# Performance work log

Measured on AMD Instinct MI355X. Metric: run time of the kernel, lower is better.

## Reference

```python
import math
import jax, jax.numpy as jnp
import numpy as np

HID = 256; NH = 8; DH = 32; DFF = 1024  # int(4.0*256)
N = 10000; E = 160000; NV = 128; NG = 64


def _ln(x, eps=1e-6):
    m = jnp.mean(x, axis=-1, keepdims=True)
    v = jnp.mean((x - m) ** 2, axis=-1, keepdims=True)
    return (x - m) * jax.lax.rsqrt(v + eps)


def _modulate(x, shift, scale):
    return x * (1.0 + scale) + shift


def _swiglu(x, W12, Wout):
    a, b = jnp.split(x @ W12, 2, axis=-1)
    return (jax.nn.silu(a) * b) @ Wout


def _adaln(t, W, b):
    return jnp.split(jax.nn.silu(t) @ W + b, 6, axis=-1)


def setup_inputs() -> dict:
    key = jax.random.key(0)
    ks = jax.random.split(key, 32)
    rn = lambda k, shape, s=1.0: jax.random.normal(k, shape, jnp.float32) * s
    W = 0.02
    return {
        "batch": jnp.sort(jax.random.randint(ks[0], (N,), 0, NG)),
        "x": rn(ks[1], (N, HID)),
        "t_emb_h": rn(ks[2], (N, HID)),
        "edge_attr": rn(ks[3], (E, HID)),
        "edge_index": jax.random.randint(ks[4], (2, E), 0, N),
        "t_emb_e": rn(ks[5], (E, HID)),
        "dist": rn(ks[6], (E, NV)),
        "W_edge_emb": rn(ks[7], (HID + NV, HID), W),
        "b_edge_emb": jnp.zeros((HID,), jnp.float32),
        "W_adaln": rn(ks[8], (HID, 6 * HID), W),
        "b_adaln": jnp.zeros((6 * HID,), jnp.float32),
        "W_adaln_e": rn(ks[9], (HID, 6 * HID), W),
        "b_adaln_e": jnp.zeros((6 * HID,), jnp.float32),
        "W_qkv": rn(ks[10], (HID, 3 * HID), W),
        "W_e0": rn(ks[11], (HID, HID), W),
        "W_e1": rn(ks[12], (HID, HID), W),
        "W_n2e": rn(ks[13], (HID, HID), W),
        "b_n2e": jnp.zeros((HID,), jnp.float32),
        "g_ln": jnp.ones((HID,), jnp.float32),
        "b_ln": jnp.zeros((HID,), jnp.float32),
        "W_ffn12": rn(ks[14], (HID, 2 * DFF), W),
        "W_ffn_out": rn(ks[15], (DFF, HID), W),
        "W_ffne12": rn(ks[16], (HID, 2 * DFF), W),
        "W_ffne_out": rn(ks[17], (DFF, HID), W),
    }


def reference(batch, x, t_emb_h, edge_attr, edge_index, t_emb_e, dist,
              W_edge_emb, b_edge_emb, W_adaln, b_adaln, W_adaln_e, b_adaln_e,
              W_qkv, W_e0, W_e1, W_n2e, b_n2e, g_ln, b_ln,
              W_ffn12, W_ffn_out, W_ffne12, W_ffne_out):
    src, tgt = edge_index[0], edge_index[1]
    n = x.shape[0]
    h_in_node = x
    h_in_edge = edge_attr

    shift_msa, scale_msa, gate_msa, shift_mlp, scale_mlp, gate_mlp = _adaln(t_emb_h, W_adaln, b_adaln)
    e_shift_msa, e_scale_msa, e_gate_msa, e_shift_mlp, e_scale_mlp, e_gate_mlp = _adaln(t_emb_e, W_adaln_e, b_adaln_e)

    edge_attr_e = jnp.concatenate([edge_attr, dist], axis=-1) @ W_edge_emb + b_edge_emb
    x_mod = _modulate(_ln(x), shift_msa, scale_msa)
    prev_edge_attr = edge_attr_e
    e_mod = _modulate(_ln(edge_attr_e), e_shift_msa, e_scale_msa)

    qkv = x_mod @ W_qkv                         # N x 3H
    Q, K, V = jnp.split(qkv, 3, axis=-1)
    Q = Q.reshape(-1, NH, DH)
    K = K.reshape(-1, NH, DH)
    V = V.reshape(-1, NH, DH)

    query_i = Q[src]                            # E x NH x DH
    key_j = K[tgt]
    value_j = V[tgt]
    edge_attn = jax.nn.gelu(e_mod @ W_e0, approximate=True).reshape(-1, NH, DH)

    alpha = jnp.sum(query_i * key_j * edge_attn, axis=-1) / math.sqrt(DH)  # E x NH
    # segment softmax over edges grouped by target node
    amax = jax.ops.segment_max(alpha, tgt, num_segments=n)                 # N x NH
    exp_a = jnp.exp(alpha - amax[tgt])
    denom = jax.ops.segment_sum(exp_a, tgt, num_segments=n)
    alpha = exp_a / denom[tgt]

    msg = value_j * (e_mod @ W_e1).reshape(-1, NH, DH) * alpha[..., None]
    out = jax.ops.segment_sum(msg.reshape(-1, NH * DH), tgt, num_segments=n)  # N x H

    h_node = out
    h_edge = (h_node[src] + h_node[tgt]) @ W_n2e + b_n2e

    h_node = h_in_node + gate_msa * h_node
    h_node = _modulate(_ln(h_node) * g_ln + b_ln, shift_mlp, scale_mlp)
    h_out = h_node + gate_mlp * _swiglu(h_node, W_ffn12, W_ffn_out)

    h_edge = h_in_edge + e_gate_msa * h_edge
    h_edge = _modulate(_ln(h_edge), e_shift_mlp, e_scale_mlp)
    h_edge_out = prev_edge_attr + h_edge + e_gate_mlp * _swiglu(h_edge, W_ffne12, W_ffne_out)
    return (h_out, h_edge_out)
```

## Files before the change

kernel.cpp:

```cpp
#include <hip/hip_runtime.h>

#define HID 256

typedef unsigned short u16;
typedef __attribute__((ext_vector_type(8))) short bf16x8;
typedef __attribute__((ext_vector_type(4))) float f32x4;

__device__ __forceinline__ float siluf(float x) { return x / (1.f + __expf(-x)); }
__device__ __forceinline__ float geluf(float x) {
    return x / (1.f + __expf(-(1.59576912f * x + 0.07135481f * x * x * x)));
}
__device__ __forceinline__ u16 f2b(float x) {
    unsigned u = __float_as_uint(x);
    unsigned r = u + 0x7FFFu + ((u >> 16) & 1u);
    return (u16)(r >> 16);
}
__device__ __forceinline__ float b2f(u16 h) {
    return __uint_as_float(((unsigned)h) << 16);
}
__device__ __forceinline__ void gload16(const u16* g, u16* l) {
    __builtin_amdgcn_global_load_lds(
        (const __attribute__((address_space(1))) unsigned int*)g,
        (__attribute__((address_space(3))) unsigned int*)l, 16, 0, 0);
}
__device__ __forceinline__ int imin(int a, int b) { return a < b ? a : b; }

__global__ __launch_bounds__(256) void gemm_mfma(
    const u16* __restrict__ A, int lda,
    const u16* __restrict__ Bt, int ldb,
    void* __restrict__ Cv, int ldc,
    int M, int N, int K,
    const float* __restrict__ bias, int act, int obf16)
{
    __shared__ u16 lds[8192];

    const int tid  = threadIdx.x;
    const int lane = tid & 63;
    const int wave = tid >> 6;
    const int row0 = blockIdx.y * 64;
    const int col0 = blockIdx.x * 128;
    const int wm   = (wave >> 1) * 32;
    const int wn   = (wave & 1) * 64;

    f32x4 acc[2][4];
#pragma unroll
    for (int i = 0; i < 2; ++i)
#pragma unroll
        for (int j = 0; j < 4; ++j) acc[i][j] = (f32x4)0.0f;

    const int kc = (lane & 3) * 8;
    const int rr  = wave * 16 + (lane >> 2);
    const int rb1 = (wave + 4) * 16 + (lane >> 2);
    const u16* pa  = A + (size_t)imin(row0 + rr, M - 1) * lda + kc;
    const u16* pb0 = Bt + (size_t)(col0 + rr) * ldb + kc;
    const u16* pb1 = Bt + (size_t)(col0 + rb1) * ldb + kc;
    u16* la  = &lds[wave * 512];
    u16* lb0 = &lds[2048 + wave * 512];
    u16* lb1 = &lds[2048 + (wave + 4) * 512];

    const int kb = (lane >> 4) * 8;
    const int fr = lane & 15;

    for (int k0 = 0; k0 < K; k0 += 32) {
        gload16(pa + k0, la);
        gload16(pb0 + k0, lb0);
        gload16(pb1 + k0, lb1);
        __syncthreads();

        bf16x8 af[2], bfm[4];
#pragma unroll
        for (int i = 0; i < 2; ++i)
            af[i] = *(const bf16x8*)&lds[(wm + i * 16 + fr) * 32 + kb];
#pragma unroll
        for (int j = 0; j < 4; ++j)
            bfm[j] = *(const bf16x8*)&lds[2048 + (wn + j * 16 + fr) * 32 + kb];
#pragma unroll
        for (int i = 0; i < 2; ++i)
#pragma unroll
            for (int j = 0; j < 4; ++j)
                acc[i][j] = __builtin_amdgcn_mfma_f32_16x16x32_bf16(af[i], bfm[j], acc[i][j], 0, 0, 0);
        __syncthreads();
    }

    const int qr = (lane >> 4) * 4;
    if (obf16) {
#pragma unroll
        for (int i = 0; i < 2; ++i)
#pragma unroll
            for (int r = 0; r < 4; ++r)
#pragma unroll
                for (int j = 0; j < 4; ++j) {
                    int lcol = wn + j * 16 + fr;
                    int gcol = col0 + lcol;
                    float v = acc[i][j][r];
                    if (bias) v += bias[gcol];
                    if (act == 2) v = geluf(v);
                    else if (act == 1) v = siluf(v);
                    else if (act == 4 && gcol < 256) v = geluf(v);
                    lds[(wm + i * 16 + qr + r) * 128 + lcol] = f2b(v);
                }
        __syncthreads();
        int row = tid >> 2, cc0 = (tid & 3) * 32;
        int grow = row0 + row;
        if (grow < M) {
            uint4* dst = (uint4*)((u16*)Cv + (size_t)grow * ldc + col0 + cc0);
            const uint4* sp = (const uint4*)&lds[row * 128 + cc0];
            dst[0] = sp[0]; dst[1] = sp[1]; dst[2] = sp[2]; dst[3] = sp[3];
        }
    } else {
        float* Cf = (float*)Cv;
#pragma unroll
        for (int i = 0; i < 2; ++i)
#pragma unroll
            for (int r = 0; r < 4; ++r) {
                int grow = row0 + wm + i * 16 + qr + r;
                if (grow >= M) continue;
#pragma unroll
                for (int j = 0; j < 4; ++j) {
                    int gcol = col0 + wn + j * 16 + fr;
                    float v = acc[i][j][r];
                    if (bias) v += bias[gcol];
                    if (act == 2) v = geluf(v);
                    else if (act == 1) v = siluf(v);
                    Cf[(size_t)grow * ldc + gcol] = v;
                }
            }
    }
}

__global__ __launch_bounds__(256) void gemm_ffn12(
    const u16* __restrict__ A, const u16* __restrict__ Wt,
    u16* __restrict__ C, int M)
{
    __shared__ u16 sm[6144];
    u16* lsA = sm;
    u16* lsB1 = sm + 2048;
    u16* lsB2 = sm + 4096;

    const int tid  = threadIdx.x;
    const int lane = tid & 63;
    const int wave = tid >> 6;
    const int row0 = blockIdx.y * 64;
    const int col0 = blockIdx.x * 64;
    const int wm   = (wave >> 1) * 32;
    const int wn   = (wave & 1) * 32;

    f32x4 accA[2][2], accB[2][2];
#pragma unroll
    for (int i = 0; i < 2; ++i)
#pragma unroll
        for (int j = 0; j < 2; ++j) { accA[i][j] = (f32x4)0.0f; accB[i][j] = (f32x4)0.0f; }

    const int kc = (lane & 3) * 8;
    const int rr = wave * 16 + (lane >> 2);
    const u16* pa  = A + (size_t)imin(row0 + rr, M - 1) * 256 + kc;
    const u16* pb1 = Wt + (size_t)(col0 + rr) * 256 + kc;
    const u16* pb2 = Wt + (size_t)(1024 + col0 + rr) * 256 + kc;
    u16* la  = &lsA[wave * 512];
    u16* lb1 = &lsB1[wave * 512];
    u16* lb2 = &lsB2[wave * 512];

    const int kb = (lane >> 4) * 8;
    const int fr = lane & 15;

#pragma unroll 1
    for (int k0 = 0; k0 < 256; k0 += 32) {
        gload16(pa + k0, la);
        gload16(pb1 + k0, lb1);
        gload16(pb2 + k0, lb2);
        __syncthreads();

        bf16x8 af[2], b1f[2], b2f_[2];
#pragma unroll
        for (int i = 0; i < 2; ++i)
            af[i] = *(const bf16x8*)&lsA[(wm + i * 16 + fr) * 32 + kb];
#pragma unroll
        for (int j = 0; j < 2; ++j) {
            b1f[j] = *(const bf16x8*)&lsB1[(wn + j * 16 + fr) * 32 + kb];
            b2f_[j] = *(const bf16x8*)&lsB2[(wn + j * 16 + fr) * 32 + kb];
        }
#pragma unroll
        for (int i = 0; i < 2; ++i)
#pragma unroll
            for (int j = 0; j < 2; ++j) {
                accA[i][j] = __builtin_amdgcn_mfma_f32_16x16x32_bf16(af[i], b1f[j], accA[i][j], 0, 0, 0);
                accB[i][j] = __builtin_amdgcn_mfma_f32_16x16x32_bf16(af[i], b2f_[j], accB[i][j], 0, 0, 0);
            }
        __syncthreads();
    }

    const int qr = (lane >> 4) * 4;
#pragma unroll
    for (int i = 0; i < 2; ++i)
#pragma unroll
        for (int r = 0; r < 4; ++r)
#pragma unroll
            for (int j = 0; j < 2; ++j) {
                float a = accA[i][j][r], b = accB[i][j][r];
                sm[(wm + i * 16 + qr + r) * 64 + wn + j * 16 + fr] = f2b(siluf(a) * b);
            }
    __syncthreads();
    int row = tid >> 2, cc0 = (tid & 3) * 16;
    int grow = row0 + row;
    if (grow < M) {
        uint4* dst = (uint4*)(C + (size_t)grow * 1024 + col0 + cc0);
        const uint4* sp = (const uint4*)&sm[row * 64 + cc0];
        dst[0] = sp[0]; dst[1] = sp[1];
    }
}

__global__ __launch_bounds__(256) void gemm_out_final(
    const u16* __restrict__ A, const u16* __restrict__ Bt,
    const float* __restrict__ eae, const u16* __restrict__ h2,
    const u16* __restrict__ gate, int ldg, int goff,
    float* __restrict__ out, int M)
{
    __shared__ u16 lds[6144];

    const int tid  = threadIdx.x;
    const int lane = tid & 63;
    const int wave = tid >> 6;
    const int row0 = blockIdx.y * 64;
    const int col0 = blockIdx.x * 128;
    const int wm   = (wave >> 1) * 32;
    const int wn   = (wave & 1) * 64;

    f32x4 acc[2][4];
#pragma unroll
    for (int i = 0; i < 2; ++i)
#pragma unroll
        for (int j = 0; j < 4; ++j) acc[i][j] = (f32x4)0.0f;

    const int kc = (lane & 3) * 8;
    const int rr = wave * 16 + (lane >> 2);
    const int rb0 = wave * 16 + (lane >> 2), rb1 = (wave + 4) * 16 + (lane >> 2);
    const u16* pa  = A + (size_t)imin(row0 + rr, M - 1) * 1024 + kc;
    const u16* pb0 = Bt + (size_t)(col0 + rb0) * 1024 + kc;
    const u16* pb1 = Bt + (size_t)(col0 + rb1) * 1024 + kc;
    u16* la  = &lds[wave * 512];
    u16* lb0 = &lds[2048 + wave * 512];
    u16* lb1 = &lds[2048 + (wave + 4) * 512];

    const int kb = (lane >> 4) * 8;
    const int fr = lane & 15;

#pragma unroll 1
    for (int k0 = 0; k0 < 1024; k0 += 32) {
        gload16(pa + k0, la);
        gload16(pb0 + k0, lb0);
        gload16(pb1 + k0, lb1);
        __syncthreads();

        bf16x8 af[2], bfm[4];
#pragma unroll
        for (int i = 0; i < 2; ++i)
            af[i] = *(const bf16x8*)&lds[(wm + i * 16 + fr) * 32 + kb];
#pragma unroll
        for (int j = 0; j < 4; ++j)
            bfm[j] = *(const bf16x8*)&lds[2048 + (wn + j * 16 + fr) * 32 + kb];
#pragma unroll
        for (int i = 0; i < 2; ++i)
#pragma unroll
            for (int j = 0; j < 4; ++j)
                acc[i][j] = __builtin_amdgcn_mfma_f32_16x16x32_bf16(af[i], bfm[j], acc[i][j], 0, 0, 0);
        __syncthreads();
    }

    const int qr = (lane >> 4) * 4;
#pragma unroll
    for (int i = 0; i < 2; ++i)
#pragma unroll
        for (int r = 0; r < 4; ++r) {
            int grow = row0 + wm + i * 16 + qr + r;
            if (grow >= M) continue;
#pragma unroll
            for (int j = 0; j < 4; ++j) {
                int gcol = col0 + wn + j * 16 + fr;
                size_t idx = (size_t)grow * 256 + gcol;
                float v = acc[i][j][r] * b2f(gate[(size_t)grow * ldg + goff + gcol]) + b2f(h2[idx]);
                if (eae) v += eae[idx];
                out[idx] = v;
            }
        }
}

__global__ __launch_bounds__(256) void k_wconv(
    const float* __restrict__ W, u16* __restrict__ Wt, int K, int N)
{
    int i = blockIdx.x * 256 + threadIdx.x;
    if (i >= K * N) return;
    int n = i / K, k = i - n * K;
    Wt[i] = f2b(W[(size_t)k * N + n]);
}

__global__ __launch_bounds__(256) void k_silu_b16(
    const float* __restrict__ src, u16* __restrict__ dst, long long n4)
{
    long long i = (long long)blockIdx.x * 256 + threadIdx.x;
    if (i >= n4) return;
    float4 v = ((const float4*)src)[i];
    ushort4 o;
    o.x = f2b(siluf(v.x)); o.y = f2b(siluf(v.y)); o.z = f2b(siluf(v.z)); o.w = f2b(siluf(v.w));
    ((ushort4*)dst)[i] = o;
}

__global__ __launch_bounds__(256) void k_pack_ed(
    const float* __restrict__ ea_, const float* __restrict__ dist,
    u16* __restrict__ out, long long cnt4)
{
    long long i = (long long)blockIdx.x * 256 + threadIdx.x;
    if (i >= cnt4) return;
    long long r = i / 96;
    int c4 = (int)(i - r * 96) * 4;
    float4 v = (c4 < 256) ? *(const float4*)(ea_ + r * 256 + c4)
                          : *(const float4*)(dist + r * 128 + (c4 - 256));
    ushort4 o;
    o.x = f2b(v.x); o.y = f2b(v.y); o.z = f2b(v.z); o.w = f2b(v.w);
    *(ushort4*)(out + r * 384 + c4) = o;
}

__global__ __launch_bounds__(256) void k_ln_mod_b16(
    const float* __restrict__ X, u16* __restrict__ Y, int M,
    const u16* __restrict__ ssb, int ldss, int shoff, int scoff)
{
    int row = (blockIdx.x << 2) + (threadIdx.x >> 6);
    if (row >= M) return;
    int lane = threadIdx.x & 63;
    const float* xr = X + (size_t)row * HID + lane * 4;
    float x0 = xr[0], x1 = xr[1], x2 = xr[2], x3 = xr[3];
    float s = x0 + x1 + x2 + x3;
    float q = x0 * x0 + x1 * x1 + x2 * x2 + x3 * x3;
#pragma unroll
    for (int o = 32; o; o >>= 1) { s += __shfl_xor(s, o, 64); q += __shfl_xor(q, o, 64); }
    float m = s * (1.f / HID);
    float r = rsqrtf(q * (1.f / HID) - m * m + 1e-6f);
    const u16* sp = ssb + (size_t)row * ldss;
    ushort4 sh = *(const ushort4*)(sp + shoff + lane * 4);
    ushort4 sc = *(const ushort4*)(sp + scoff + lane * 4);
    ushort4 o;
    o.x = f2b((x0 - m) * r * (1.f + b2f(sc.x)) + b2f(sh.x));
    o.y = f2b((x1 - m) * r * (1.f + b2f(sc.y)) + b2f(sh.y));
    o.z = f2b((x2 - m) * r * (1.f + b2f(sc.z)) + b2f(sh.z));
    o.w = f2b((x3 - m) * r * (1.f + b2f(sc.w)) + b2f(sh.w));
    ((ushort4*)(Y + (size_t)row * HID))[lane] = o;
}

__global__ __launch_bounds__(256) void k_ln_mod_resid_b16(
    const float* __restrict__ A, const float* __restrict__ Bv, u16* __restrict__ Y, int M,
    const u16* __restrict__ gb, int ldg, int goff,
    const u16* __restrict__ ssb, int ldss, int shoff, int scoff,
    const float* __restrict__ gw, const float* __restrict__ bw)
{
    int row = (blockIdx.x << 2) + (threadIdx.x >> 6);
    if (row >= M) return;
    int lane = threadIdx.x & 63;
    const float* ar = A + (size_t)row * HID + lane * 4;
    const float* br = Bv + (size_t)row * HID + lane * 4;
    ushort4 gp = *(const ushort4*)(gb + (size_t)row * ldg + goff + lane * 4);
    float t0 = ar[0] + b2f(gp.x) * br[0];
    float t1 = ar[1] + b2f(gp.y) * br[1];
    float t2 = ar[2] + b2f(gp.z) * br[2];
    float t3 = ar[3] + b2f(gp.w) * br[3];
    float s = t0 + t1 + t2 + t3;
    float q = t0 * t0 + t1 * t1 + t2 * t2 + t3 * t3;
#pragma unroll
    for (int o = 32; o; o >>= 1) { s += __shfl_xor(s, o, 64); q += __shfl_xor(q, o, 64); }
    float m = s * (1.f / HID);
    float r = rsqrtf(q * (1.f / HID) - m * m + 1e-6f);
    float n0 = (t0 - m) * r, n1 = (t1 - m) * r, n2 = (t2 - m) * r, n3 = (t3 - m) * r;
    if (gw) {
        const float* g4 = gw + lane * 4;
        const float* b4 = bw + lane * 4;
        n0 = n0 * g4[0] + b4[0]; n1 = n1 * g4[1] + b4[1];
        n2 = n2 * g4[2] + b4[2]; n3 = n3 * g4[3] + b4[3];
    }
    const u16* sp = ssb + (size_t)row * ldss;
    ushort4 sh = *(const ushort4*)(sp + shoff + lane * 4);
    ushort4 sc = *(const ushort4*)(sp + scoff + lane * 4);
    ushort4 o;
    o.x = f2b(n0 * (1.f + b2f(sc.x)) + b2f(sh.x));
    o.y = f2b(n1 * (1.f + b2f(sc.y)) + b2f(sh.y));
    o.z = f2b(n2 * (1.f + b2f(sc.z)) + b2f(sh.z));
    o.w = f2b(n3 * (1.f + b2f(sc.w)) + b2f(sh.w));
    ((ushort4*)(Y + (size_t)row * HID))[lane] = o;
}

__device__ __forceinline__ unsigned fkey(float f) {
    unsigned u = __float_as_uint(f);
    return (u & 0x80000000u) ? ~u : (u | 0x80000000u);
}
__device__ __forceinline__ float funkey(unsigned k) {
    return (k & 0x80000000u) ? __uint_as_float(k & 0x7FFFFFFFu) : __uint_as_float(~k);
}

__global__ __launch_bounds__(256) void attn_alpha_k(
    const u16* __restrict__ qkv, const u16* __restrict__ ea, int lde,
    const int* __restrict__ src, const int* __restrict__ tgt,
    float* __restrict__ alpha, unsigned* __restrict__ amaxU)
{
    int e = blockIdx.x;
    int t = threadIdx.x;
    int h = t >> 5, d = t & 31;
    int s = src[e], g = tgt[e];
    float qv = b2f(qkv[(size_t)s * 768 + h * 32 + d]);
    float kv = b2f(qkv[(size_t)g * 768 + 256 + h * 32 + d]);
    float wv = b2f(ea[(size_t)e * lde + t]);
    float v = qv * kv * wv;
#pragma unroll
    for (int o = 16; o; o >>= 1) v += __shfl_xor(v, o, 32);
    if (d == 0) {
        float a = v * 0.17677669529663687f;
        alpha[(size_t)e * 8 + h] = a;
        atomicMax(&amaxU[(size_t)g * 8 + h], fkey(a));
    }
}

__global__ __launch_bounds__(256) void attn_exp_k(
    float* __restrict__ alpha, const unsigned* __restrict__ amaxU,
    float* __restrict__ denom, const int* __restrict__ tgt, int EH)
{
    int i = blockIdx.x * 256 + threadIdx.x;
    if (i >= EH) return;
    int e = i >> 3, h = i & 7;
    int g = tgt[e];
    float m = funkey(amaxU[(size_t)g * 8 + h]);
    float ex = __expf(alpha[i] - m);
    alpha[i] = ex;
    atomicAdd(&denom[(size_t)g * 8 + h], ex);
}

__global__ __launch_bounds__(256) void attn_msg_k(
    const u16* __restrict__ qkv, const u16* __restrict__ ea1,
    const float* __restrict__ alpha, const float* __restrict__ denom,
    const int* __restrict__ tgt, float* __restrict__ hattn, long long EC)
{
    long long i = (long long)blockIdx.x * 256 + threadIdx.x;
    if (i >= EC) return;
    long long e = i >> 8;
    int c = (int)(i & 255);
    int h = c >> 5;
    int g = tgt[e];
    float w = alpha[e * 8 + h] / denom[(size_t)g * 8 + h];
    float val = b2f(qkv[(size_t)g * 768 + 512 + c]) * b2f(ea1[e * 512 + 256 + c]) * w;
    atomicAdd(&hattn[(size_t)g * 256 + c], val);
}

__global__ __launch_bounds__(256) void k_gsum_b16(
    const float* __restrict__ hattn, const int* __restrict__ src, const int* __restrict__ tgt,
    u16* __restrict__ g, long long cnt4)
{
    long long i = (long long)blockIdx.x * 256 + threadIdx.x;
    if (i >= cnt4) return;
    long long e = i >> 6;
    int c4 = (int)(i & 63) * 4;
    float4 a = *(const float4*)(hattn + (size_t)src[e] * 256 + c4);
    float4 b = *(const float4*)(hattn + (size_t)tgt[e] * 256 + c4);
    ushort4 o;
    o.x = f2b(a.x + b.x); o.y = f2b(a.y + b.y); o.z = f2b(a.z + b.z); o.w = f2b(a.w + b.w);
    ((ushort4*)g)[i] = o;
}

static inline void gemm(hipStream_t st, const u16* A, int lda, const u16* Bt, int ldb,
                        void* C, int ldc, int M, int N, int K,
                        const float* bias, int act, int obf16)
{
    dim3 g(N / 128, (M + 63) / 64);
    hipLaunchKernelGGL(gemm_mfma, g, dim3(256), 0, st, A, lda, Bt, ldb, C, ldc, M, N, K,
                       bias, act, obf16);
}

extern "C" void kernel_launch(void* const* d_in, const int* in_sizes, int n_in,
                              void* d_out, int out_size, void* d_ws, size_t ws_size,
                              hipStream_t stream)
{
    const int Nn = in_sizes[0];
    const int E = in_sizes[3] / HID;

    const float* x        = (const float*)d_in[1];
    const float* t_emb_h  = (const float*)d_in[2];
    const float* edge_attr= (const float*)d_in[3];
    const int*   eidx     = (const int*)d_in[4];
    const float* t_emb_e  = (const float*)d_in[5];
    const float* dist     = (const float*)d_in[6];
    const float* W_ee     = (const float*)d_in[7];
    const float* b_ee     = (const float*)d_in[8];
    const float* W_ad     = (const float*)d_in[9];
    const float* b_ad     = (const float*)d_in[10];
    const float* W_ade    = (const float*)d_in[11];
    const float* b_ade    = (const float*)d_in[12];
    const float* W_qkv    = (const float*)d_in[13];
    const float* W_e0     = (const float*)d_in[14];
    const float* W_e1     = (const float*)d_in[15];
    const float* W_n2e    = (const float*)d_in[16];
    const float* b_n2e    = (const float*)d_in[17];
    const float* g_ln     = (const float*)d_in[18];
    const float* b_ln     = (const float*)d_in[19];
    const float* W_f12    = (const float*)d_in[20];
    const float* W_fout   = (const float*)d_in[21];
    const float* W_fe12   = (const float*)d_in[22];
    const float* W_feout  = (const float*)d_in[23];

    const int* src = eidx;
    const int* tgt = eidx + E;

    float* outN = (float*)d_out;
    float* outE = (float*)d_out + (size_t)Nn * 256;

    char* W = (char*)d_ws;
    size_t off = 0;
    auto alloc = [&](size_t bytes) -> size_t {
        size_t o = off; off += (bytes + 255) & ~(size_t)255; return o;
    };
    float*    alpha = (float*)(W + alloc((size_t)E * 8 * 4));
    unsigned* amaxU = (unsigned*)(W + alloc((size_t)Nn * 8 * 4));
    float*    den   = (float*)(W + alloc((size_t)Nn * 8 * 4));
    float*    hat   = (float*)(W + alloc((size_t)Nn * 256 * 4));
    u16*      qkvb  = (u16*)(W + alloc((size_t)Nn * 768 * 2));
    u16*      sth   = (u16*)(W + alloc((size_t)Nn * 256 * 2));
    u16*      steb  = (u16*)(W + alloc((size_t)E * 256 * 2));
    u16*      ea1b  = (u16*)(W + alloc((size_t)E * 512 * 2));
    u16*      adnb  = (u16*)(W + alloc((size_t)Nn * 1536 * 2));
    u16*      xmb   = (u16*)(W + alloc((size_t)Nn * 256 * 2));
    u16*      h2nb  = (u16*)(W + alloc((size_t)Nn * 256 * 2));
    u16*      cnb   = (u16*)(W + alloc((size_t)Nn * 1024 * 2));
    u16* weet   = (u16*)(W + alloc((size_t)256 * 384 * 2));
    u16* wadt   = (u16*)(W + alloc((size_t)1536 * 256 * 2));
    u16* wadet  = (u16*)(W + alloc((size_t)1536 * 256 * 2));
    u16* wqkvt  = (u16*)(W + alloc((size_t)768 * 256 * 2));
    u16* we01t  = (u16*)(W + alloc((size_t)512 * 256 * 2));
    u16* wn2et  = (u16*)(W + alloc((size_t)256 * 256 * 2));
    u16* wf12t  = (u16*)(W + alloc((size_t)2048 * 256 * 2));
    u16* wfoutt = (u16*)(W + alloc((size_t)256 * 1024 * 2));
    u16* wfe12t = (u16*)(W + alloc((size_t)2048 * 256 * 2));
    u16* wfeoutt= (u16*)(W + alloc((size_t)256 * 1024 * 2));

    char* pool = W + off;
    size_t poolB = (ws_size > off) ? (ws_size - off) : 0;
    auto chunkRowsB = [&](size_t bytesPerRow, int total) -> int {
        long c = (long)(poolB / bytesPerRow);
        c = (c / 256) * 256;
        if (c < 256) c = 256;
        if (c > total) c = (long)total;
        return (int)c;
    };

    hipMemsetAsync(amaxU, 0, (size_t)Nn * 8 * 4, stream);
    hipMemsetAsync(den, 0, (size_t)Nn * 8 * 4, stream);
    hipMemsetAsync(hat, 0, (size_t)Nn * 256 * 4, stream);

    {
        struct WC { const float* w; u16* wt; int K, N; } wl[] = {
            { W_ee,    weet,   384, 256 },
            { W_ad,    wadt,   256, 1536 },
            { W_ade,   wadet,  256, 1536 },
            { W_qkv,   wqkvt,  256, 768 },
            { W_e0,    we01t,  256, 256 },
            { W_e1,    we01t + 256 * 256, 256, 256 },
            { W_n2e,   wn2et,  256, 256 },
            { W_f12,   wf12t,  256, 2048 },
            { W_fout,  wfoutt, 1024, 256 },
            { W_fe12,  wfe12t, 256, 2048 },
            { W_feout, wfeoutt,1024, 256 },
        };
        for (auto& e : wl) {
            int cnt = e.K * e.N;
            hipLaunchKernelGGL(k_wconv, dim3((cnt + 255) / 256), dim3(256), 0, stream,
                               e.w, e.wt, e.K, e.N);
        }
    }

    hipLaunchKernelGGL(k_silu_b16, dim3((unsigned)(((long long)Nn * 64 + 255) / 256)), dim3(256),
                       0, stream, t_emb_h, sth, (long long)Nn * 64);
    hipLaunchKernelGGL(k_silu_b16, dim3((unsigned)(((long long)E * 64 + 255) / 256)), dim3(256),
                       0, stream, t_emb_e, steb, (long long)E * 64);

    gemm(stream, sth, 256, wadt, 256, adnb, 1536, Nn, 1536, 256, b_ad, 0, 1);
    hipLaunchKernelGGL(k_ln_mod_b16, dim3((Nn + 3) / 4), dim3(256), 0, stream,
                       x, xmb, Nn, adnb, 1536, 0, 256);
    gemm(stream, xmb, 256, wqkvt, 256, qkvb, 768, Nn, 768, 256, nullptr, 0, 1);

    {
        int C = chunkRowsB(1536 + 1024 + 512, E);
        char* p = pool;
        u16* eab2 = (u16*)p; p += (size_t)C * 1536;
        u16* emsb = (u16*)p; p += (size_t)C * 1024;
        u16* emod = (u16*)p;
        for (int s = 0; s < E; s += C) {
            int cc = (E - s < C) ? (E - s) : C;
            float* eaeC = outE + (size_t)s * 256;
            hipLaunchKernelGGL(k_pack_ed, dim3((unsigned)(((long long)cc * 96 + 255) / 256)),
                               dim3(256), 0, stream, edge_attr + (size_t)s * 256,
                               dist + (size_t)s * 128, eab2, (long long)cc * 96);
            gemm(stream, eab2, 384, weet, 384, eaeC, 256, cc, 256, 384, b_ee, 0, 0);
            gemm(stream, steb + (size_t)s * 256, 256, wadet, 256, emsb, 512, cc, 512, 256,
                 b_ade, 0, 1);
            hipLaunchKernelGGL(k_ln_mod_b16, dim3((cc + 3) / 4), dim3(256), 0, stream,
                               eaeC, emod, cc, emsb, 512, 0, 256);
            gemm(stream, emod, 256, we01t, 256, ea1b + (size_t)s * 512, 512, cc, 512, 256,
                 nullptr, 4, 1);
            hipLaunchKernelGGL(attn_alpha_k, dim3(cc), dim3(256), 0, stream,
                               qkvb, ea1b + (size_t)s * 512, 512, src + s, tgt + s,
                               alpha + (size_t)s * 8, amaxU);
        }
    }

    hipLaunchKernelGGL(attn_exp_k, dim3((E * 8 + 255) / 256), dim3(256), 0, stream,
                       alpha, amaxU, den, tgt, E * 8);

    hipLaunchKernelGGL(attn_msg_k, dim3((unsigned)(((long long)E * 256 + 255) / 256)), dim3(256),
                       0, stream, qkvb, ea1b, alpha, den, tgt, hat, (long long)E * 256);

    hipLaunchKernelGGL(k_ln_mod_resid_b16, dim3((Nn + 3) / 4), dim3(256), 0, stream,
                       x, hat, h2nb, Nn, adnb, 1536, 512, adnb, 1536, 768, 1024, g_ln, b_ln);
    hipLaunchKernelGGL(gemm_ffn12, dim3(16, (Nn + 63) / 64), dim3(256), 0, stream,
                       h2nb, wf12t, cnb, Nn);
    hipLaunchKernelGGL(gemm_out_final, dim3(2, (Nn + 63) / 64), dim3(256), 0, stream,
                       cnb, wfoutt, (const float*)nullptr, h2nb, adnb, 1536, 1280, outN, Nn);

    {
        int C = chunkRowsB(512 + 2048 + 1024 + 512 + 2048, E);
        char* p = pool;
        u16*   gsum = (u16*)p;  p += (size_t)C * 512;
        u16*   em2b = (u16*)p;  p += (size_t)C * 2048;
        float* hep  = (float*)p; p += (size_t)C * 1024;
        u16*   h2e  = (u16*)p;  p += (size_t)C * 512;
        u16*   cne  = (u16*)p;
        for (int s = 0; s < E; s += C) {
            int cc = (E - s < C) ? (E - s) : C;
            hipLaunchKernelGGL(k_gsum_b16, dim3((unsigned)(((long long)cc * 64 + 255) / 256)),
                               dim3(256), 0, stream, hat, src + s, tgt + s, gsum, (long long)cc * 64);
            gemm(stream, gsum, 256, wn2et, 256, hep, 256, cc, 256, 256, b_n2e, 0, 0);
            gemm(stream, steb + (size_t)s * 256, 256, wadet + 512 * 256, 256, em2b, 1024,
                 cc, 1024, 256, b_ade + 512, 0, 1);
            hipLaunchKernelGGL(k_ln_mod_resid_b16, dim3((cc + 3) / 4), dim3(256), 0, stream,
                               edge_attr + (size_t)s * 256, hep, h2e, cc,
                               em2b, 1024, 0, em2b, 1024, 256, 512, nullptr, nullptr);
            hipLaunchKernelGGL(gemm_ffn12, dim3(16, (cc + 63) / 64), dim3(256), 0, stream,
                               h2e, wfe12t, cne, cc);
            hipLaunchKernelGGL(gemm_out_final, dim3(2, (cc + 63) / 64), dim3(256), 0, stream,
                               cne, wfeoutt, outE + (size_t)s * 256, h2e,
                               em2b, 1024, 768, outE + (size_t)s * 256, cc);
        }
    }
    (void)n_in; (void)out_size;
}
```

Before: 2.278 ms.

## Replace atomic segment softmax and scatter with CSR-by-target gather reductions

Builds a CSR grouping of edges by target node with histogram, scan and scatter kernels. The segment max and denominator, and the message aggregation, then become per-node gather loops instead of atomicMax/atomicAdd scatters over E×256 elements. V[tgt] is factored out of the per-edge sum because it is constant within a segment. This removes heavy float-atomic contention on hattn, at the cost of extra preprocessing kernels, a single-block serial scan, and irregular per-node loop lengths.

Result: faster. 2.234 ms (-2.0%).

```diff
diff --git a/kernel.cpp b/kernel.cpp
--- a/kernel.cpp
+++ b/kernel.cpp
@@ -385,18 +385,10 @@
     ((ushort4*)(Y + (size_t)row * HID))[lane] = o;
 }
 
-__device__ __forceinline__ unsigned fkey(float f) {
-    unsigned u = __float_as_uint(f);
-    return (u & 0x80000000u) ? ~u : (u | 0x80000000u);
-}
-__device__ __forceinline__ float funkey(unsigned k) {
-    return (k & 0x80000000u) ? __uint_as_float(k & 0x7FFFFFFFu) : __uint_as_float(~k);
-}
-
 __global__ __launch_bounds__(256) void attn_alpha_k(
     const u16* __restrict__ qkv, const u16* __restrict__ ea, int lde,
     const int* __restrict__ src, const int* __restrict__ tgt,
-    float* __restrict__ alpha, unsigned* __restrict__ amaxU)
+    float* __restrict__ alpha)
 {
     int e = blockIdx.x;
     int t = threadIdx.x;
@@ -408,41 +400,94 @@
     float v = qv * kv * wv;
 #pragma unroll
     for (int o = 16; o; o >>= 1) v += __shfl_xor(v, o, 32);
-    if (d == 0) {
-        float a = v * 0.17677669529663687f;
-        alpha[(size_t)e * 8 + h] = a;
-        atomicMax(&amaxU[(size_t)g * 8 + h], fkey(a));
-    }
-}
-
-__global__ __launch_bounds__(256) void attn_exp_k(
-    float* __restrict__ alpha, const unsigned* __restrict__ amaxU,
-    float* __restrict__ denom, const int* __restrict__ tgt, int EH)
+    if (d == 0) alpha[(size_t)e * 8 + h] = v * 0.17677669529663687f;
+}
+
+__global__ __launch_bounds__(256) void k_hist(
+    const int* __restrict__ tgt, int* __restrict__ counts, int E)
+{
+    int i = blockIdx.x * 256 + threadIdx.x;
+    if (i < E) atomicAdd(&counts[tgt[i]], 1);
+}
+
+__global__ __launch_bounds__(256) void k_scan(
+    const int* __restrict__ counts, int* __restrict__ offsets, int Nn)
+{
+    __shared__ int part[256];
+    __shared__ int pref[257];
+    int t = threadIdx.x;
+    int chunk = (Nn + 255) / 256;
+    int lo = t * chunk, hi = imin(lo + chunk, Nn);
+    int s = 0;
+    for (int i = lo; i < hi; ++i) s += counts[i];
+    part[t] = s;
+    __syncthreads();
+    if (t == 0) {
+        int run = 0;
+        for (int i = 0; i < 256; ++i) { pref[i] = run; run += part[i]; }
+        pref[256] = run;
+        offsets[Nn] = run;
+    }
+    __syncthreads();
+    int run = pref[t];
+    for (int i = lo; i < hi; ++i) { offsets[i] = run; run += counts[i]; }
+}
+
+__global__ __launch_bounds__(256) void k_scatter(
+    const int* __restrict__ tgt, int* __restrict__ cursor,
+    int* __restrict__ eidlist, int E)
+{
+    int i = blockIdx.x * 256 + threadIdx.x;
+    if (i < E) {
+        int pos = atomicAdd(&cursor[tgt[i]], 1);
+        eidlist[pos] = i;
+    }
+}
+
+__global__ __launch_bounds__(256) void k_amax_den(
+    const float* __restrict__ alpha, const int* __restrict__ offsets,
+    const int* __restrict__ eidlist, float* __restrict__ amaxF,
+    float* __restrict__ invden, int NH8)
+{
+    int i = blockIdx.x * 256 + threadIdx.x;
+    if (i >= NH8) return;
+    int n = i >> 3, h = i & 7;
+    int b = offsets[n], e = offsets[n + 1];
+    float m = -1e30f;
+    for (int k = b; k < e; ++k) m = fmaxf(m, alpha[(size_t)eidlist[k] * 8 + h]);
+    float s = 0.f;
+    for (int k = b; k < e; ++k) s += __expf(alpha[(size_t)eidlist[k] * 8 + h] - m);
+    amaxF[i] = m;
+    invden[i] = (s > 0.f) ? 1.f / s : 0.f;
+}
+
+__global__ __launch_bounds__(256) void k_norm(
+    float* __restrict__ alpha, const float* __restrict__ amaxF,
+    const float* __restrict__ invden, const int* __restrict__ tgt, int EH)
 {
     int i = blockIdx.x * 256 + threadIdx.x;
     if (i >= EH) return;
     int e = i >> 3, h = i & 7;
     int g = tgt[e];
-    float m = funkey(amaxU[(size_t)g * 8 + h]);
-    float ex = __expf(alpha[i] - m);
-    alpha[i] = ex;
-    atomicAdd(&denom[(size_t)g * 8 + h], ex);
-}
-
-__global__ __launch_bounds__(256) void attn_msg_k(
+    alpha[i] = __expf(alpha[i] - amaxF[(size_t)g * 8 + h]) * invden[(size_t)g * 8 + h];
+}
+
+__global__ __launch_bounds__(256) void attn_msg_csr(
     const u16* __restrict__ qkv, const u16* __restrict__ ea1,
-    const float* __restrict__ alpha, const float* __restrict__ denom,
-    const int* __restrict__ tgt, float* __restrict__ hattn, long long EC)
-{
-    long long i = (long long)blockIdx.x * 256 + threadIdx.x;
-    if (i >= EC) return;
-    long long e = i >> 8;
-    int c = (int)(i & 255);
+    const float* __restrict__ alpha, const int* __restrict__ offsets,
+    const int* __restrict__ eidlist, float* __restrict__ hattn)
+{
+    int n = blockIdx.x;
+    int c = threadIdx.x;
     int h = c >> 5;
-    int g = tgt[e];
-    float w = alpha[e * 8 + h] / denom[(size_t)g * 8 + h];
-    float val = b2f(qkv[(size_t)g * 768 + 512 + c]) * b2f(ea1[e * 512 + 256 + c]) * w;
-    atomicAdd(&hattn[(size_t)g * 256 + c], val);
+    int b = offsets[n], e = offsets[n + 1];
+    float acc = 0.f;
+    for (int k = b; k < e; ++k) {
+        int eid = eidlist[k];
+        float w = alpha[(size_t)eid * 8 + h];
+        acc += b2f(ea1[(size_t)eid * 512 + 256 + c]) * w;
+    }
+    hattn[(size_t)n * 256 + c] = b2f(qkv[(size_t)n * 768 + 512 + c]) * acc;
 }
 
 __global__ __launch_bounds__(256) void k_gsum_b16(
@@ -512,9 +557,12 @@
         size_t o = off; off += (bytes + 255) & ~(size_t)255; return o;
     };
     float*    alpha = (float*)(W + alloc((size_t)E * 8 * 4));
-    unsigned* amaxU = (unsigned*)(W + alloc((size_t)Nn * 8 * 4));
-    float*    den   = (float*)(W + alloc((size_t)Nn * 8 * 4));
+    float*    amaxF = (float*)(W + alloc((size_t)Nn * 8 * 4));
+    float*    invden= (float*)(W + alloc((size_t)Nn * 8 * 4));
     float*    hat   = (float*)(W + alloc((size_t)Nn * 256 * 4));
+    int*      offs  = (int*)(W + alloc((size_t)(Nn + 1) * 4));
+    int*      cursor= (int*)(W + alloc((size_t)Nn * 4));
+    int*      eidl  = (int*)(W + alloc((size_t)E * 4));
     u16*      qkvb  = (u16*)(W + alloc((size_t)Nn * 768 * 2));
     u16*      sth   = (u16*)(W + alloc((size_t)Nn * 256 * 2));
     u16*      steb  = (u16*)(W + alloc((size_t)E * 256 * 2));
@@ -544,9 +592,12 @@
         return (int)c;
     };
 
-    hipMemsetAsync(amaxU, 0, (size_t)Nn * 8 * 4, stream);
-    hipMemsetAsync(den, 0, (size_t)Nn * 8 * 4, stream);
-    hipMemsetAsync(hat, 0, (size_t)Nn * 256 * 4, stream);
+    hipMemsetAsync(cursor, 0, (size_t)Nn * 4, stream);
+    hipLaunchKernelGGL(k_hist, dim3((E + 255) / 256), dim3(256), 0, stream, tgt, cursor, E);
+    hipLaunchKernelGGL(k_scan, dim3(1), dim3(256), 0, stream, cursor, offs, Nn);
+    hipMemcpyAsync(cursor, offs, (size_t)Nn * 4, hipMemcpyDeviceToDevice, stream);
+    hipLaunchKernelGGL(k_scatter, dim3((E + 255) / 256), dim3(256), 0, stream,
+                       tgt, cursor, eidl, E);
 
     {
         struct WC { const float* w; u16* wt; int K, N; } wl[] = {
@@ -600,15 +651,17 @@
                  nullptr, 4, 1);
             hipLaunchKernelGGL(attn_alpha_k, dim3(cc), dim3(256), 0, stream,
                                qkvb, ea1b + (size_t)s * 512, 512, src + s, tgt + s,
-                               alpha + (size_t)s * 8, amaxU);
+                               alpha + (size_t)s * 8);
         }
     }
 
-    hipLaunchKernelGGL(attn_exp_k, dim3((E * 8 + 255) / 256), dim3(256), 0, stream,
-                       alpha, amaxU, den, tgt, E * 8);
-
-    hipLaunchKernelGGL(attn_msg_k, dim3((unsigned)(((long long)E * 256 + 255) / 256)), dim3(256),
-                       0, stream, qkvb, ea1b, alpha, den, tgt, hat, (long long)E * 256);
+    hipLaunchKernelGGL(k_amax_den, dim3((Nn * 8 + 255) / 256), dim3(256), 0, stream,
+                       alpha, offs, eidl, amaxF, invden, Nn * 8);
+    hipLaunchKernelGGL(k_norm, dim3((E * 8 + 255) / 256), dim3(256), 0, stream,
+                       alpha, amaxF, invden, tgt, E * 8);
+
+    hipLaunchKernelGGL(attn_msg_csr, dim3(Nn), dim3(256), 0, stream,
+                       qkvb, ea1b, alpha, offs, eidl, hat);
 
     hipLaunchKernelGGL(k_ln_mod_resid_b16, dim3((Nn + 3) / 4), dim3(256), 0, stream,
                        x, hat, h2nb, Nn, adnb, 1536, 512, adnb, 1536, 768, 1024, g_ln, b_ln);
```
